# Kernel optimization log

Measured on AMD Instinct MI355X. Metric: run time of the kernel, lower is better.

Reference implementation:

```python
import jax, jax.numpy as jnp
import numpy as np

SEQ_LEN = 4096
D_IN = 2048
D_OUT = 2048
DROPOUT_P = 0.5


def setup_inputs() -> dict:
    key = jax.random.key(0)
    kx, kq, kk, kv = jax.random.split(key, 4)
    return {
        "x": jax.random.normal(kx, (SEQ_LEN, D_IN), dtype=jnp.float32),
        "W_query": jax.random.uniform(kq, (D_IN, D_OUT), dtype=jnp.float32),
        "W_key": jax.random.uniform(kk, (D_IN, D_OUT), dtype=jnp.float32),
        "W_value": jax.random.uniform(kv, (D_IN, D_OUT), dtype=jnp.float32),
    }


def reference(x, W_query, W_key, W_value):
    # projections: [S, d_in] @ [d_in, d_out] -> [S, d_out]
    queries = x @ W_query
    keys = x @ W_key
    values = x @ W_value
    # full score matrix [S, S]
    attn_scores = queries @ keys.T
    S = attn_scores.shape[0]
    causal_mask = jnp.triu(jnp.ones((S, S), dtype=bool), k=1)
    masked = jnp.where(causal_mask, -jnp.inf, attn_scores)
    scale = jnp.sqrt(jnp.asarray(keys.shape[-1], dtype=masked.dtype))
    attn_weights = jax.nn.softmax(masked / scale, axis=1)
    # dropout p=0.5 (train mode), inverted scaling, deterministic key
    keep = jax.random.bernoulli(jax.random.key(42), 1.0 - DROPOUT_P, attn_weights.shape)
    attn_weights = jnp.where(keep, attn_weights / (1.0 - DROPOUT_P), 0.0)
    context_vec = attn_weights @ values  # [S, d_out]
    return context_vec
```

## Files before the change

### kernel.cpp

```cpp
#include <hip/hip_runtime.h>
#include <cstdint>
#include <cstddef>
#include <cmath>

#define SEQ 4096
#define DM  2048

typedef unsigned int u32;
typedef unsigned short u16;
typedef __attribute__((ext_vector_type(8))) short bf16x8;
typedef __attribute__((ext_vector_type(4))) float f32x4;
typedef __attribute__((ext_vector_type(16))) float f32x16;

__device__ __forceinline__ u16 f2bf(float f) {
  u32 u = __float_as_uint(f);
  return (u16)((u + 0x7FFFu + ((u >> 16) & 1u)) >> 16);
}
__device__ __forceinline__ float bf2f(u16 h) { return __uint_as_float(((u32)h) << 16); }

__device__ __forceinline__ u32 rotl32(u32 x, int r) { return (x << r) | (x >> (32 - r)); }

__device__ __forceinline__ void tf2x32(u32 c0, u32 c1, u32& o0, u32& o1) {
  const u32 k0 = 0u, k1 = 42u, k2 = 0x1BD11BDAu ^ 0u ^ 42u;
  u32 x0 = c0 + k0;
  u32 x1 = c1 + k1;
#define TFR(r) { x0 += x1; x1 = rotl32(x1, (r)); x1 ^= x0; }
  TFR(13) TFR(15) TFR(26) TFR(6)   x0 += k1; x1 += k2 + 1u;
  TFR(17) TFR(29) TFR(16) TFR(24)  x0 += k2; x1 += k0 + 2u;
  TFR(13) TFR(15) TFR(26) TFR(6)   x0 += k0; x1 += k1 + 3u;
  TFR(17) TFR(29) TFR(16) TFR(24)  x0 += k1; x1 += k2 + 4u;
  TFR(13) TFR(15) TFR(26) TFR(6)   x0 += k2; x1 += k0 + 5u;
#undef TFR
  o0 = x0; o1 = x1;
}

__device__ __forceinline__ bool dropout_keep(u32 idx) {
  u32 a, b; tf2x32(0u, idx, a, b);
  return (((a ^ b) & 0x80000000u) == 0u);
}

__device__ __forceinline__ void g2l16(const void* g, void* l) {
  __builtin_amdgcn_global_load_lds((const __attribute__((address_space(1))) u32*)g,
                                   (__attribute__((address_space(3))) u32*)l, 16, 0, 0);
}

#define MFMA16(a, b, c) __builtin_amdgcn_mfma_f32_16x16x32_bf16(a, b, c, 0, 0, 0)
#define MFMA32(a, b, c) __builtin_amdgcn_mfma_f32_32x32x16_bf16(a, b, c, 0, 0, 0)


__device__ __forceinline__ void gemm_core(
    const u16* __restrict__ Ah, const u16* __restrict__ Bh,
    int lda, int ldb, int rowBlock, int colBlock, int kmax,
    f32x4 (&acc)[4][4], u16* smem)
{
  u16* Als = smem;
  u16* Bls = smem + 8192;
  const int tid  = threadIdx.x;
  const int wid  = tid >> 6;
  const int lane = tid & 63;
  const int wr   = (wid & 1) << 6;
  const int wc   = (wid >> 1) << 6;
  const int lrow = lane & 15;
  const int lk   = (((lane >> 4) ^ ((lrow >> 1) & 3)) << 3);
  const int srow = wid * 32 + (lane >> 2);
  const int skol = (((lane & 3) ^ ((lane >> 3) & 3)) << 3);

  const f32x4 zero = {0.f, 0.f, 0.f, 0.f};
#pragma unroll
  for (int i = 0; i < 4; ++i)
#pragma unroll
    for (int j = 0; j < 4; ++j) acc[i][j] = zero;

  for (int kb = 0; kb < kmax; kb += 64) {
#pragma unroll
    for (int h = 0; h < 2; ++h)
#pragma unroll
      for (int t = 0; t < 2; ++t) {
        const size_t ga = (size_t)(rowBlock + srow + t * 16) * lda + kb + h * 32 + skol;
        const size_t gb = (size_t)(colBlock + srow + t * 16) * ldb + kb + h * 32 + skol;
        const int lo = h * 4096 + (wid * 32 + t * 16) * 32;
        g2l16(Ah + ga, &Als[lo]);
        g2l16(Bh + gb, &Bls[lo]);
      }
    __syncthreads();

#pragma unroll
    for (int h = 0; h < 2; ++h) {
      bf16x8 ah[4], bh[4];
#pragma unroll
      for (int r = 0; r < 4; ++r) {
        ah[r] = *(const bf16x8*)&Als[h * 4096 + (wr + r * 16 + lrow) * 32 + lk];
        bh[r] = *(const bf16x8*)&Bls[h * 4096 + (wc + r * 16 + lrow) * 32 + lk];
      }
#pragma unroll
      for (int r = 0; r < 4; ++r)
#pragma unroll
        for (int c = 0; c < 4; ++c)
          acc[r][c] = MFMA16(ah[r], bh[c], acc[r][c]);
    }
    __syncthreads();
  }
}

__global__ __launch_bounds__(256) void k_split_all(
    const float* __restrict__ X, u16* __restrict__ Xh, u16* __restrict__ Xl,
    const float* __restrict__ Wq, const float* __restrict__ Wk, const float* __restrict__ Wv,
    u16* __restrict__ Wqh, u16* __restrict__ Wql,
    u16* __restrict__ Wkh, u16* __restrict__ Wkl, u16* __restrict__ Wvh) {
  __shared__ float t[64][65];
  const int bid = blockIdx.x;
  const int tid = threadIdx.x;
  const int wid = tid >> 6, lane = tid & 63;

  if (bid < 4096) {
    const int kt16 = bid & 127;
    const int rt32 = (bid >> 7) * 4 + wid;
    const int row = rt32 * 32 + (lane & 31);
    const int col = kt16 * 16 + ((lane >> 5) << 3);
    const float* src = X + (size_t)row * DM + col;
    const float4 v0 = *(const float4*)src;
    const float4 v1 = *(const float4*)(src + 4);
    float v[8] = {v0.x, v0.y, v0.z, v0.w, v1.x, v1.y, v1.z, v1.w};
    u16 h[8], l[8];
#pragma unroll
    for (int j = 0; j < 8; ++j) {
      h[j] = f2bf(v[j]);
      l[j] = f2bf(v[j] - bf2f(h[j]));
    }
    u16* hp = Xh + (size_t)row * DM + col;
    *(ushort4*)hp = *(ushort4*)&h[0];
    *(ushort4*)(hp + 4) = *(ushort4*)&h[4];
    u16* lp = Xl + (((size_t)rt32 * 128 + kt16) * 64 + lane) * 8;
    *(ushort4*)lp = *(ushort4*)&l[0];
    *(ushort4*)(lp + 4) = *(ushort4*)&l[4];
    return;
  }

  const int r = bid - 4096;
  const int z = r >> 10;
  const int rem = r & 1023;
  const int n0 = (rem & 31) * 64, k0 = (rem >> 5) * 64;
  const float* W = (z == 0) ? Wq : (z == 1) ? Wk : Wv;
  u16* Oh = (z == 0) ? Wqh : (z == 1) ? Wkh : Wvh;
  u16* Ol = (z == 0) ? Wql : Wkl;
  const int tx = tid & 63, ty = tid >> 6;
#pragma unroll
  for (int i = 0; i < 16; ++i)
    t[ty * 16 + i][tx] = W[(size_t)(k0 + ty * 16 + i) * DM + n0 + tx];
  __syncthreads();
  {
    const int nl = tid >> 2, kc = (tid & 3) * 16;
    u16 h[16];
#pragma unroll
    for (int i = 0; i < 16; ++i) h[i] = f2bf(t[kc + i][nl]);
    u16* hp = Oh + (size_t)(n0 + nl) * DM + k0 + kc;
#pragma unroll
    for (int i = 0; i < 4; ++i) *(ushort4*)(hp + i * 4) = *(ushort4*)&h[i * 4];
  }
  if (z < 2) {
#pragma unroll
    for (int tt = 0; tt < 2; ++tt) {
      const int idx = wid * 2 + tt;
      const int rt = idx >> 2, kt = idx & 3;
      const int nl = rt * 32 + (lane & 31);
      const int kc = kt * 16 + ((lane >> 5) << 3);
      u16 l[8];
#pragma unroll
      for (int j = 0; j < 8; ++j) {
        const float v = t[kc + j][nl];
        l[j] = f2bf(v - bf2f(f2bf(v)));
      }
      const int rtg = (n0 >> 5) + rt, ktg = (k0 >> 4) + kt;
      u16* lp = Ol + (((size_t)rtg * (DM / 16) + ktg) * 64 + lane) * 8;
      *(ushort4*)lp = *(ushort4*)&l[0];
      *(ushort4*)(lp + 4) = *(ushort4*)&l[4];
    }
  }
}

__global__ __launch_bounds__(512, 2) void k_proj_qk(
    const u16* __restrict__ Xh, const u16* __restrict__ Xl,
    const u16* __restrict__ Wqh, const u16* __restrict__ Wql,
    const u16* __restrict__ Wkh, const u16* __restrict__ Wkl,
    u16* __restrict__ Qh, u16* __restrict__ Ql,
    u16* __restrict__ Kh, u16* __restrict__ Kl, float rscaleQ)
{
  __shared__ __align__(16) u16 smem[65536];
  const int z = blockIdx.z;
  const u16* __restrict__ Bw = z ? Wkh : Wqh;
  const u16* __restrict__ Bl = z ? Wkl : Wql;
  u16* __restrict__ Oh = z ? Kh : Qh;
  u16* __restrict__ Ol = z ? Kl : Ql;
  const float rs = z ? 1.0f : rscaleQ;

  const int rowBlock = blockIdx.y * 256;
  const int colBlock = blockIdx.x * 256;
  const int tid  = threadIdx.x;
  const int wid  = tid >> 6, lane = tid & 63;
  const int wm   = wid >> 2, wn = wid & 3;
  const int l31  = lane & 31, lh = lane >> 5;
  const int srow = tid >> 2, schunk = tid & 3;
  const int sko  = ((schunk ^ ((srow >> 1) & 3)) << 3);
  const int rkey = (l31 >> 1) & 3;

  f32x16 acc[4][2];
  {
    const f32x16 z16 = {0.f,0.f,0.f,0.f,0.f,0.f,0.f,0.f,0.f,0.f,0.f,0.f,0.f,0.f,0.f,0.f};
#pragma unroll
    for (int r = 0; r < 4; ++r)
#pragma unroll
      for (int c = 0; c < 2; ++c) acc[r][c] = z16;
  }

#define P_STG_AHI(pp) g2l16(Xh + (size_t)(rowBlock + (pp)*128 + srow) * DM + kbn + sko, \
                            &smem[bufN + (pp)*4096 + tid*8]);
#define P_STG_BHI(pp) g2l16(Bw + (size_t)(colBlock + (pp)*128 + srow) * DM + kbn + sko, \
                            &smem[bufN + 8192 + (pp)*4096 + tid*8]);
#define P_STG_ALO(ss) { const int idx_ = (ss)*8 + wid; \
    g2l16(Xl + ((size_t)((rowBlock >> 5) + (idx_ >> 1)) * 128 + (kbn >> 4) + (idx_ & 1)) * 512 + lane*8, \
          &smem[bufN + 16384 + idx_*512 + lane*8]); }
#define P_STG_BLO(ss) { const int idx_ = (ss)*8 + wid; \
    g2l16(Bl + ((size_t)((colBlock >> 5) + (idx_ >> 1)) * 128 + (kbn >> 4) + (idx_ & 1)) * 512 + lane*8, \
          &smem[bufN + 24576 + idx_*512 + lane*8]); }

#define P_PHASE(qq) { \
    bf16x8 ah[4], bh[2], al[4], bl[2]; \
    const int cl_ = (qq)*2 + lh; \
    _Pragma("unroll") for (int r_ = 0; r_ < 4; ++r_) \
      ah[r_] = *(const bf16x8*)&smem[bufC + ((wm*128 + r_*32 + l31) << 5) + ((cl_ ^ rkey) << 3)]; \
    _Pragma("unroll") for (int c_ = 0; c_ < 2; ++c_) \
      bh[c_] = *(const bf16x8*)&smem[bufC + 8192 + ((wn*64 + c_*32 + l31) << 5) + ((cl_ ^ rkey) << 3)]; \
    _Pragma("unroll") for (int r_ = 0; r_ < 4; ++r_) \
      al[r_] = *(const bf16x8*)&smem[bufC + 16384 + ((wm*4 + r_)*2 + (qq))*512 + lane*8]; \
    _Pragma("unroll") for (int c_ = 0; c_ < 2; ++c_) \
      bl[c_] = *(const bf16x8*)&smem[bufC + 24576 + ((wn*2 + c_)*2 + (qq))*512 + lane*8]; \
    __builtin_amdgcn_s_setprio(1); \
    _Pragma("unroll") for (int r_ = 0; r_ < 4; ++r_) \
      _Pragma("unroll") for (int c_ = 0; c_ < 2; ++c_) { \
        acc[r_][c_] = MFMA32(ah[r_], bh[c_], acc[r_][c_]); \
        acc[r_][c_] = MFMA32(ah[r_], bl[c_], acc[r_][c_]); \
        acc[r_][c_] = MFMA32(al[r_], bh[c_], acc[r_][c_]); } \
    __builtin_amdgcn_s_setprio(0); }

  {
    const size_t kbn = 0; const int bufN = 0;
    P_STG_AHI(0) P_STG_AHI(1) P_STG_BHI(0) P_STG_BHI(1)
    P_STG_ALO(0) P_STG_ALO(1) P_STG_BLO(0) P_STG_BLO(1)
  }
  asm volatile("s_waitcnt vmcnt(0)" ::: "memory");
  __builtin_amdgcn_s_barrier();

  for (int t = 0; t < 64; ++t) {
    const int bufC = (t & 1) << 15;
    const int bufN = bufC ^ 32768;
    const size_t kbn = (size_t)(t + 1) * 32;
    if (t < 63) { P_STG_AHI(0) P_STG_AHI(1) P_STG_BHI(0) P_STG_BHI(1) }
    __builtin_amdgcn_sched_barrier(0);
    P_PHASE(0)
    if (t < 63) { P_STG_ALO(0) P_STG_ALO(1) P_STG_BLO(0) P_STG_BLO(1) }
    __builtin_amdgcn_sched_barrier(0);
    P_PHASE(1)
    asm volatile("s_waitcnt vmcnt(0)" ::: "memory");
    __builtin_amdgcn_s_barrier();
  }
#undef P_PHASE
#undef P_STG_BLO
#undef P_STG_ALO
#undef P_STG_BHI
#undef P_STG_AHI

  __syncthreads();
  u16* scr = smem + wid * 8192;
  const int r0g = rowBlock + wm * 128;
  const int c0g = colBlock + wn * 64;
#pragma unroll
  for (int r = 0; r < 4; ++r)
#pragma unroll
    for (int c = 0; c < 2; ++c) {
      const int colL = c * 32 + l31;
#pragma unroll
      for (int g = 0; g < 4; ++g)
#pragma unroll
        for (int e = 0; e < 4; ++e) {
          const int rowL = r * 32 + 8 * g + 4 * lh + e;
          const float v = acc[r][c][g * 4 + e] * rs;
          const u16 h = f2bf(v);
          Oh[(size_t)(r0g + rowL) * DM + c0g + colL] = h;
          scr[rowL * 64 + (((colL >> 3) ^ (rowL & 7)) << 3) + (colL & 7)] =
              f2bf(v - bf2f(h));
        }
    }
  asm volatile("s_waitcnt lgkmcnt(0)" ::: "memory");
  __builtin_amdgcn_sched_barrier(0);
#pragma unroll
  for (int rt = 0; rt < 4; ++rt)
#pragma unroll
    for (int kt = 0; kt < 4; ++kt) {
      const int rowL = rt * 32 + l31;
      const int cl2 = kt * 2 + lh;
      const bf16x8 v = *(const bf16x8*)&scr[rowL * 64 + ((cl2 ^ (rowL & 7)) << 3)];
      const int rtg = (rowBlock >> 5) + wm * 4 + rt;
      const int ktg = (colBlock >> 4) + wn * 4 + kt;
      *(bf16x8*)(Ol + (((size_t)rtg * 128 + ktg) * 64 + lane) * 8) = v;
    }
}

__global__ __launch_bounds__(512, 2) void k_proj_v(
    const u16* __restrict__ Xh, const u16* __restrict__ Wvh, u16* __restrict__ Vt)
{
  __shared__ __align__(16) u16 smem[49152];
  const int rowBlock = blockIdx.y * 256;
  const int colBlock = blockIdx.x * 128;
  const int tid  = threadIdx.x;
  const int wid  = tid >> 6, lane = tid & 63;
  const int wm   = wid >> 1, wn = wid & 1;
  const int l31  = lane & 31, lh = lane >> 5;
  const int srow = tid >> 2, schunk = tid & 3;
  const int sko  = ((schunk ^ ((srow >> 1) & 3)) << 3);
  const int rkey = (l31 >> 1) & 3;

  f32x16 acc[2][2];
  {
    const f32x16 z16 = {0.f,0.f,0.f,0.f,0.f,0.f,0.f,0.f,0.f,0.f,0.f,0.f,0.f,0.f,0.f,0.f};
#pragma unroll
    for (int r = 0; r < 2; ++r)
#pragma unroll
      for (int c = 0; c < 2; ++c) acc[r][c] = z16;
  }

#define V_STGA(hh, pp) g2l16(Xh + (size_t)(rowBlock + (pp)*128 + srow) * DM + kbn + (hh)*32 + sko, \
                             &smem[bufN + (hh)*8192 + (pp)*4096 + tid*8]);
#define V_STGB(hh)     g2l16(Wvh + (size_t)(colBlock + srow) * DM + kbn + (hh)*32 + sko, \
                             &smem[bufN + 16384 + (hh)*4096 + tid*8]);

#define V_PH(qq, STMT) { \
    __builtin_amdgcn_sched_barrier(0); \
    STMT; \
    bf16x8 ah[2], bh[2]; \
    const int cl_ = ((qq) & 1) * 2 + lh; \
    const int hx_ = (qq) >> 1; \
    _Pragma("unroll") for (int r_ = 0; r_ < 2; ++r_) \
      ah[r_] = *(const bf16x8*)&smem[bufC + ((hx_*256 + wm*64 + r_*32 + l31) << 5) + ((cl_ ^ rkey) << 3)]; \
    _Pragma("unroll") for (int c_ = 0; c_ < 2; ++c_) \
      bh[c_] = *(const bf16x8*)&smem[bufC + 16384 + ((hx_*128 + wn*64 + c_*32 + l31) << 5) + ((cl_ ^ rkey) << 3)]; \
    __builtin_amdgcn_s_setprio(1); \
    _Pragma("unroll") for (int r_ = 0; r_ < 2; ++r_) \
      _Pragma("unroll") for (int c_ = 0; c_ < 2; ++c_) \
        acc[r_][c_] = MFMA32(ah[r_], bh[c_], acc[r_][c_]); \
    __builtin_amdgcn_s_setprio(0); }

  {
    const size_t kbn = 0; const int bufN = 0;
    V_STGA(0,0) V_STGA(0,1) V_STGA(1,0) V_STGA(1,1) V_STGB(0) V_STGB(1)
  }
  asm volatile("s_waitcnt vmcnt(0)" ::: "memory");
  __builtin_amdgcn_s_barrier();

  for (int t = 0; t < 32; ++t) {
    const int bufC = (t & 1) * 24576;
    const int bufN = bufC ^ 24576;
    const size_t kbn = (size_t)(t + 1) * 64;
    const bool more = (t < 31);
    V_PH(0, if (more) { V_STGA(0,0) V_STGA(0,1) V_STGB(0) })
    V_PH(1, if (more) { V_STGA(1,0) V_STGA(1,1) V_STGB(1) })
    V_PH(2, ;)
    V_PH(3, ;)
    asm volatile("s_waitcnt vmcnt(0)" ::: "memory");
    __builtin_amdgcn_s_barrier();
  }
#undef V_PH
#undef V_STGB
#undef V_STGA

  const int vr0 = rowBlock + wm * 64;
#pragma unroll
  for (int r = 0; r < 2; ++r)
#pragma unroll
    for (int c = 0; c < 2; ++c) {
      const int col = colBlock + wn * 64 + c * 32 + l31;
#pragma unroll
      for (int g = 0; g < 4; ++g) {
        ushort4 pk;
        pk.x = f2bf(acc[r][c][g * 4 + 0]);
        pk.y = f2bf(acc[r][c][g * 4 + 1]);
        pk.z = f2bf(acc[r][c][g * 4 + 2]);
        pk.w = f2bf(acc[r][c][g * 4 + 3]);
        *(ushort4*)(Vt + (size_t)col * SEQ + vr0 + r * 32 + 8 * g + 4 * lh) = pk;
      }
    }
}

__global__ __launch_bounds__(512, 2) void k_scores(
    const u16* __restrict__ Qh, const u16* __restrict__ Ql,
    const u16* __restrict__ Kh, const u16* __restrict__ Kl, float* __restrict__ S)
{
  __shared__ __align__(16) u16 smem[49152];
  const int bid = blockIdx.x;
  int by = (int)((sqrtf(4.0f * (float)bid + 1.0f) - 1.0f) * 0.5f);
  while ((by + 1) * (by + 2) <= bid) ++by;
  while (by * (by + 1) > bid) --by;
  const int bx = bid - by * (by + 1);
  const int rowBlock = by * 256, colBlock = bx * 128;

  const int tid  = threadIdx.x;
  const int wid  = tid >> 6, lane = tid & 63;
  const int wm   = wid >> 1, wn = wid & 1;
  const int l31  = lane & 31, lh = lane >> 5;
  const int srow = tid >> 2, schunk = tid & 3;
  const int sko  = ((schunk ^ ((srow >> 1) & 3)) << 3);
  const int rkey = (l31 >> 1) & 3;

  f32x16 acc[2][2];
  {
    const f32x16 z16 = {0.f,0.f,0.f,0.f,0.f,0.f,0.f,0.f,0.f,0.f,0.f,0.f,0.f,0.f,0.f,0.f};
#pragma unroll
    for (int r = 0; r < 2; ++r)
#pragma unroll
      for (int c = 0; c < 2; ++c) acc[r][c] = z16;
  }

#define S_STG_AHI(pp) g2l16(Qh + (size_t)(rowBlock + (pp)*128 + srow) * DM + kbn + sko, \
                            &smem[bufN + (pp)*4096 + tid*8]);
#define S_STG_BHI     g2l16(Kh + (size_t)(colBlock + srow) * DM + kbn + sko, \
                            &smem[bufN + 8192 + tid*8]);
#define S_STG_ALO(ss) { const int idx_ = (ss)*8 + wid; \
    g2l16(Ql + ((size_t)((rowBlock >> 5) + (idx_ >> 1)) * 128 + (kbn >> 4) + (idx_ & 1)) * 512 + lane*8, \
          &smem[bufN + 12288 + idx_*512 + lane*8]); }
#define S_STG_BLO     { const int idx_ = wid; \
    g2l16(Kl + ((size_t)((colBlock >> 5) + (idx_ >> 1)) * 128 + (kbn >> 4) + (idx_ & 1)) * 512 + lane*8, \
          &smem[bufN + 20480 + idx_*512 + lane*8]); }

#define S_PHASE(qq) { \
    bf16x8 ah[2], bh[2], al[2], bl[2]; \
    const int cl_ = (qq)*2 + lh; \
    _Pragma("unroll") for (int r_ = 0; r_ < 2; ++r_) \
      ah[r_] = *(const bf16x8*)&smem[bufC + ((wm*64 + r_*32 + l31) << 5) + ((cl_ ^ rkey) << 3)]; \
    _Pragma("unroll") for (int c_ = 0; c_ < 2; ++c_) \
      bh[c_] = *(const bf16x8*)&smem[bufC + 8192 + ((wn*64 + c_*32 + l31) << 5) + ((cl_ ^ rkey) << 3)]; \
    _Pragma("unroll") for (int r_ = 0; r_ < 2; ++r_) \
      al[r_] = *(const bf16x8*)&smem[bufC + 12288 + ((wm*2 + r_)*2 + (qq))*512 + lane*8]; \
    _Pragma("unroll") for (int c_ = 0; c_ < 2; ++c_) \
      bl[c_] = *(const bf16x8*)&smem[bufC + 20480 + ((wn*2 + c_)*2 + (qq))*512 + lane*8]; \
    __builtin_amdgcn_s_setprio(1); \
    _Pragma("unroll") for (int r_ = 0; r_ < 2; ++r_) \
      _Pragma("unroll") for (int c_ = 0; c_ < 2; ++c_) { \
        acc[r_][c_] = MFMA32(ah[r_], bh[c_], acc[r_][c_]); \
        acc[r_][c_] = MFMA32(ah[r_], bl[c_], acc[r_][c_]); \
        acc[r_][c_] = MFMA32(al[r_], bh[c_], acc[r_][c_]); } \
    __builtin_amdgcn_s_setprio(0); }

  {
    const size_t kbn = 0; const int bufN = 0;
    S_STG_AHI(0) S_STG_AHI(1) S_STG_BHI
    S_STG_ALO(0) S_STG_ALO(1) S_STG_BLO
  }
  asm volatile("s_waitcnt vmcnt(0)" ::: "memory");
  __builtin_amdgcn_s_barrier();

  for (int t = 0; t < 64; ++t) {
    const int bufC = (t & 1) * 24576;
    const int bufN = bufC ^ 24576;
    const size_t kbn = (size_t)(t + 1) * 32;
    if (t < 63) { S_STG_AHI(0) S_STG_AHI(1) S_STG_BHI }
    __builtin_amdgcn_sched_barrier(0);
    S_PHASE(0)
    if (t < 63) { S_STG_ALO(0) S_STG_ALO(1) S_STG_BLO }
    __builtin_amdgcn_sched_barrier(0);
    S_PHASE(1)
    asm volatile("s_waitcnt vmcnt(0)" ::: "memory");
    __builtin_amdgcn_s_barrier();
  }
#undef S_PHASE
#undef S_STG_BLO
#undef S_STG_ALO
#undef S_STG_BHI
#undef S_STG_AHI

  const int r0 = rowBlock + wm * 64, c0 = colBlock + wn * 64;
#pragma unroll
  for (int r = 0; r < 2; ++r)
#pragma unroll
    for (int c = 0; c < 2; ++c) {
      const int col = c0 + c * 32 + l31;
#pragma unroll
      for (int g = 0; g < 4; ++g)
#pragma unroll
        for (int e = 0; e < 4; ++e) {
          const int row = r0 + r * 32 + 8 * g + 4 * lh + e;
          S[(size_t)row * SEQ + col] = acc[r][c][g * 4 + e];
        }
    }
}

__global__ __launch_bounds__(256) void k_softmax_dropout(const float* __restrict__ S,
                                                         u16* __restrict__ P) {
  const int row = blockIdx.x;
  const int n = row + 1;
  const int nt = (n + 1023) >> 10;
  const int tid = threadIdx.x;
  __shared__ float buf[SEQ];
  __shared__ float red[4];
  __shared__ float bcast;
  const float* srow = S + (size_t)row * SEQ;

  float lmax = -INFINITY;
  for (int t = 0; t < nt; ++t) {
    int j4 = tid + t * 256;
    float4 v = *(const float4*)(srow + (size_t)j4 * 4);
    int b = j4 * 4;
    float x0 = (b + 0 < n) ? v.x : -INFINITY;
    float x1 = (b + 1 < n) ? v.y : -INFINITY;
    float x2 = (b + 2 < n) ? v.z : -INFINITY;
    float x3 = (b + 3 < n) ? v.w : -INFINITY;
    buf[b + 0] = x0; buf[b + 1] = x1; buf[b + 2] = x2; buf[b + 3] = x3;
    lmax = fmaxf(lmax, fmaxf(fmaxf(x0, x1), fmaxf(x2, x3)));
  }
  for (int off = 32; off > 0; off >>= 1) lmax = fmaxf(lmax, __shfl_down(lmax, off, 64));
  if ((tid & 63) == 0) red[tid >> 6] = lmax;
  __syncthreads();
  if (tid == 0) bcast = fmaxf(fmaxf(red[0], red[1]), fmaxf(red[2], red[3]));
  __syncthreads();
  const float m = bcast;

  float lsum = 0.f;
  for (int t = 0; t < nt; ++t) {
    int b = (tid + t * 256) * 4;
    float e0 = expf(buf[b + 0] - m);
    float e1 = expf(buf[b + 1] - m);
    float e2 = expf(buf[b + 2] - m);
    float e3 = expf(buf[b + 3] - m);
    buf[b + 0] = e0; buf[b + 1] = e1; buf[b + 2] = e2; buf[b + 3] = e3;
    lsum += (e0 + e1) + (e2 + e3);
  }
  for (int off = 32; off > 0; off >>= 1) lsum += __shfl_down(lsum, off, 64);
  if ((tid & 63) == 0) red[tid >> 6] = lsum;
  __syncthreads();
  if (tid == 0) bcast = (red[0] + red[1]) + (red[2] + red[3]);
  __syncthreads();
  const float total = bcast;

  u16* prow = P + (size_t)row * SEQ;
  const int zeroEnd = ((row >> 7) + 1) << 7;
  for (int j = tid; j < zeroEnd; j += 256) {
    float out = 0.f;
    if (j < n) {
      const float w = buf[j] / total;
      out = dropout_keep((u32)(row * SEQ + j)) ? w * 2.0f : 0.f;
    }
    prow[j] = f2bf(out);
  }
}

__global__ __launch_bounds__(256) void k_pv(const u16* __restrict__ P,
                                            const u16* __restrict__ Vt,
                                            float* __restrict__ O) {
  __shared__ __align__(16) u16 smem[16384];
  const int by = (SEQ / 128 - 1) - blockIdx.y;
  f32x4 acc[4][4];
  gemm_core(P, Vt, SEQ, SEQ, by * 128, blockIdx.x * 128, (by + 1) * 128, acc, smem);

  const int lane = threadIdx.x & 63, wid = threadIdx.x >> 6;
  const int r0 = by * 128 + ((wid & 1) << 6) + ((lane >> 4) << 2);
  const int c0 = blockIdx.x * 128 + ((wid >> 1) << 6) + (lane & 15);
#pragma unroll
  for (int r = 0; r < 4; ++r)
#pragma unroll
    for (int c = 0; c < 4; ++c)
#pragma unroll
      for (int e = 0; e < 4; ++e)
        O[(size_t)(r0 + r * 16 + e) * DM + (c0 + c * 16)] = acc[r][c][e];
}

extern "C" void kernel_launch(void* const* d_in, const int* in_sizes, int n_in,
                              void* d_out, int out_size, void* d_ws, size_t ws_size,
                              hipStream_t stream) {
  const float* x  = (const float*)d_in[0];
  const float* Wq = (const float*)d_in[1];
  const float* Wk = (const float*)d_in[2];
  const float* Wv = (const float*)d_in[3];

  const size_t PL = (size_t)SEQ * DM;
  const size_t WL = (size_t)DM * DM;
  u16* base = (u16*)d_ws;
  u16* Qh = base;
  u16* Ql = Qh + PL;
  u16* Kh = Ql + PL;
  u16* Kl = Kh + PL;
  u16* Vt = Kl + PL;
  u16* P  = base;
  u16* regA = Vt + PL;
  u16* Xh  = regA;
  u16* Xl  = Xh + PL;
  u16* Wqh = Xl + PL;
  u16* Wql = Wqh + WL;
  u16* Wkh = Wql + WL;
  u16* Wkl = Wkh + WL;
  u16* Wvh = Wkl + WL;
  float* S = (float*)regA;

  const float rscale = 1.0f / sqrtf(2048.0f);
  k_split_all<<<dim3(4096 + 3 * 1024), dim3(256), 0, stream>>>(
      x, Xh, Xl, Wq, Wk, Wv, Wqh, Wql, Wkh, Wkl, Wvh);
  k_proj_qk<<<dim3(DM / 256, SEQ / 256, 2), dim3(512), 0, stream>>>(
      Xh, Xl, Wqh, Wql, Wkh, Wkl, Qh, Ql, Kh, Kl, rscale);
  k_proj_v<<<dim3(DM / 128, SEQ / 256), dim3(512), 0, stream>>>(Xh, Wvh, Vt);
  k_scores<<<dim3(272), dim3(512), 0, stream>>>(Qh, Ql, Kh, Kl, S);
  k_softmax_dropout<<<dim3(SEQ), dim3(256), 0, stream>>>(S, P);
  k_pv<<<dim3(DM / 128, SEQ / 128), dim3(256), 0, stream>>>(P, Vt, (float*)d_out);
}
```

Baseline: 610.4 us.

## Fuse V projection into scores launch, compact causal S, stream lo-parts from global

The V projection and the causal score GEMM now share one launch, with blocks beyond the score range computing V, so the two independent workloads can overlap and fill the GPU. The score matrix is stored in a packed lower-triangular layout indexed by 128-row bands, which shrinks the fp32 scratch footprint and lets it live in the Xl region. The QK projection is also restructured to stage only the high bf16 halves in shared memory with a deeper k-step, while the low halves are loaded straight from global memory into registers with double buffering. This cuts LDS traffic but adds direct global loads inside the MFMA loop.

```diff
diff --git a/kernel.cpp b/kernel.cpp
--- a/kernel.cpp
+++ b/kernel.cpp
@@ -17,6 +17,11 @@
   return (u16)((u + 0x7FFFu + ((u >> 16) & 1u)) >> 16);
 }
 __device__ __forceinline__ float bf2f(u16 h) { return __uint_as_float(((u32)h) << 16); }
+
+__device__ __forceinline__ size_t s_base(int row) {
+  const int b = row >> 7;
+  return (size_t)8192 * b * (b + 1) + (size_t)128 * (row & 127) * (b + 1);
+}
 
 __device__ __forceinline__ u32 rotl32(u32 x, int r) { return (x << r) | (x >> (32 - r)); }
 
@@ -202,6 +207,8 @@
   const int srow = tid >> 2, schunk = tid & 3;
   const int sko  = ((schunk ^ ((srow >> 1) & 3)) << 3);
   const int rkey = (l31 >> 1) & 3;
+  const int rtA0 = (rowBlock >> 5) + wm * 4;
+  const int rtB0 = (colBlock >> 5) + wn * 2;
 
   f32x16 acc[4][2];
   {
@@ -211,63 +218,65 @@
 #pragma unroll
       for (int c = 0; c < 2; ++c) acc[r][c] = z16;
   }
-
-#define P_STG_AHI(pp) g2l16(Xh + (size_t)(rowBlock + (pp)*128 + srow) * DM + kbn + sko, \
-                            &smem[bufN + (pp)*4096 + tid*8]);
-#define P_STG_BHI(pp) g2l16(Bw + (size_t)(colBlock + (pp)*128 + srow) * DM + kbn + sko, \
-                            &smem[bufN + 8192 + (pp)*4096 + tid*8]);
-#define P_STG_ALO(ss) { const int idx_ = (ss)*8 + wid; \
-    g2l16(Xl + ((size_t)((rowBlock >> 5) + (idx_ >> 1)) * 128 + (kbn >> 4) + (idx_ & 1)) * 512 + lane*8, \
-          &smem[bufN + 16384 + idx_*512 + lane*8]); }
-#define P_STG_BLO(ss) { const int idx_ = (ss)*8 + wid; \
-    g2l16(Bl + ((size_t)((colBlock >> 5) + (idx_ >> 1)) * 128 + (kbn >> 4) + (idx_ & 1)) * 512 + lane*8, \
-          &smem[bufN + 24576 + idx_*512 + lane*8]); }
-
-#define P_PHASE(qq) { \
-    bf16x8 ah[4], bh[2], al[4], bl[2]; \
-    const int cl_ = (qq)*2 + lh; \
+  bf16x8 alo0[4], blo0[2], alo1[4], blo1[2];
+
+#define QK_STG(hh, pp) { \
+    g2l16(Xh + (size_t)(rowBlock + (pp)*128 + srow) * DM + kbn + (hh)*32 + sko, \
+          &smem[bufN + (hh)*8192 + (pp)*4096 + tid*8]); \
+    g2l16(Bw + (size_t)(colBlock + (pp)*128 + srow) * DM + kbn + (hh)*32 + sko, \
+          &smem[bufN + 16384 + (hh)*8192 + (pp)*4096 + tid*8]); }
+
+#define QK_LO(AV, BV, kt) { \
+    const int kk_ = (kt); \
     _Pragma("unroll") for (int r_ = 0; r_ < 4; ++r_) \
-      ah[r_] = *(const bf16x8*)&smem[bufC + ((wm*128 + r_*32 + l31) << 5) + ((cl_ ^ rkey) << 3)]; \
+      AV[r_] = *(const bf16x8*)(Xl + (((size_t)(rtA0 + r_) * 128 + kk_) * 64 + lane) * 8); \
     _Pragma("unroll") for (int c_ = 0; c_ < 2; ++c_) \
-      bh[c_] = *(const bf16x8*)&smem[bufC + 8192 + ((wn*64 + c_*32 + l31) << 5) + ((cl_ ^ rkey) << 3)]; \
+      BV[c_] = *(const bf16x8*)(Bl + (((size_t)(rtB0 + c_) * 128 + kk_) * 64 + lane) * 8); }
+
+#define QK_PH(qq, ALC, BLC, ALN, BLN, STMT, ktn) { \
+    __builtin_amdgcn_sched_barrier(0); \
+    QK_LO(ALN, BLN, ktn); \
+    __builtin_amdgcn_sched_barrier(0); \
+    STMT; \
+    bf16x8 ah[4], bh[2]; \
+    const int cl_ = ((qq) & 1) * 2 + lh; \
+    const int hx_ = (qq) >> 1; \
     _Pragma("unroll") for (int r_ = 0; r_ < 4; ++r_) \
-      al[r_] = *(const bf16x8*)&smem[bufC + 16384 + ((wm*4 + r_)*2 + (qq))*512 + lane*8]; \
+      ah[r_] = *(const bf16x8*)&smem[bufC + ((hx_*256 + wm*128 + r_*32 + l31) << 5) + ((cl_ ^ rkey) << 3)]; \
     _Pragma("unroll") for (int c_ = 0; c_ < 2; ++c_) \
-      bl[c_] = *(const bf16x8*)&smem[bufC + 24576 + ((wn*2 + c_)*2 + (qq))*512 + lane*8]; \
+      bh[c_] = *(const bf16x8*)&smem[bufC + 16384 + ((hx_*256 + wn*64 + c_*32 + l31) << 5) + ((cl_ ^ rkey) << 3)]; \
     __builtin_amdgcn_s_setprio(1); \
     _Pragma("unroll") for (int r_ = 0; r_ < 4; ++r_) \
       _Pragma("unroll") for (int c_ = 0; c_ < 2; ++c_) { \
         acc[r_][c_] = MFMA32(ah[r_], bh[c_], acc[r_][c_]); \
-        acc[r_][c_] = MFMA32(ah[r_], bl[c_], acc[r_][c_]); \
-        acc[r_][c_] = MFMA32(al[r_], bh[c_], acc[r_][c_]); } \
+        acc[r_][c_] = MFMA32(ah[r_], BLC[c_], acc[r_][c_]); \
+        acc[r_][c_] = MFMA32(ALC[r_], bh[c_], acc[r_][c_]); } \
     __builtin_amdgcn_s_setprio(0); }
 
   {
     const size_t kbn = 0; const int bufN = 0;
-    P_STG_AHI(0) P_STG_AHI(1) P_STG_BHI(0) P_STG_BHI(1)
-    P_STG_ALO(0) P_STG_ALO(1) P_STG_BLO(0) P_STG_BLO(1)
-  }
+    QK_STG(0,0) QK_STG(0,1) QK_STG(1,0) QK_STG(1,1)
+  }
+  QK_LO(alo0, blo0, 0);
   asm volatile("s_waitcnt vmcnt(0)" ::: "memory");
   __builtin_amdgcn_s_barrier();
 
-  for (int t = 0; t < 64; ++t) {
+  for (int t = 0; t < 32; ++t) {
     const int bufC = (t & 1) << 15;
     const int bufN = bufC ^ 32768;
-    const size_t kbn = (size_t)(t + 1) * 32;
-    if (t < 63) { P_STG_AHI(0) P_STG_AHI(1) P_STG_BHI(0) P_STG_BHI(1) }
-    __builtin_amdgcn_sched_barrier(0);
-    P_PHASE(0)
-    if (t < 63) { P_STG_ALO(0) P_STG_ALO(1) P_STG_BLO(0) P_STG_BLO(1) }
-    __builtin_amdgcn_sched_barrier(0);
-    P_PHASE(1)
+    const size_t kbn = (size_t)(t + 1) * 64;
+    const bool more = (t < 31);
+    const int g4 = t * 4;
+    QK_PH(0, alo0, blo0, alo1, blo1, if (more) { QK_STG(0,0) QK_STG(0,1) }, g4 + 1)
+    QK_PH(1, alo1, blo1, alo0, blo0, if (more) { QK_STG(1,0) QK_STG(1,1) }, g4 + 2)
+    QK_PH(2, alo0, blo0, alo1, blo1, ;, g4 + 3)
+    QK_PH(3, alo1, blo1, alo0, blo0, ;, (g4 + 4 < 128 ? g4 + 4 : 127))
     asm volatile("s_waitcnt vmcnt(0)" ::: "memory");
     __builtin_amdgcn_s_barrier();
   }
-#undef P_PHASE
-#undef P_STG_BLO
-#undef P_STG_ALO
-#undef P_STG_BHI
-#undef P_STG_AHI
+#undef QK_PH
+#undef QK_LO
+#undef QK_STG
 
   __syncthreads();
   u16* scr = smem + wid * 8192;
@@ -305,96 +314,11 @@
     }
 }
 
-__global__ __launch_bounds__(512, 2) void k_proj_v(
-    const u16* __restrict__ Xh, const u16* __restrict__ Wvh, u16* __restrict__ Vt)
+__device__ __forceinline__ void scores_body(
+    const u16* __restrict__ Qh, const u16* __restrict__ Ql,
+    const u16* __restrict__ Kh, const u16* __restrict__ Kl,
+    float* __restrict__ S, u16* smem)
 {
-  __shared__ __align__(16) u16 smem[49152];
-  const int rowBlock = blockIdx.y * 256;
-  const int colBlock = blockIdx.x * 128;
-  const int tid  = threadIdx.x;
-  const int wid  = tid >> 6, lane = tid & 63;
-  const int wm   = wid >> 1, wn = wid & 1;
-  const int l31  = lane & 31, lh = lane >> 5;
-  const int srow = tid >> 2, schunk = tid & 3;
-  const int sko  = ((schunk ^ ((srow >> 1) & 3)) << 3);
-  const int rkey = (l31 >> 1) & 3;
-
-  f32x16 acc[2][2];
-  {
-    const f32x16 z16 = {0.f,0.f,0.f,0.f,0.f,0.f,0.f,0.f,0.f,0.f,0.f,0.f,0.f,0.f,0.f,0.f};
-#pragma unroll
-    for (int r = 0; r < 2; ++r)
-#pragma unroll
-      for (int c = 0; c < 2; ++c) acc[r][c] = z16;
-  }
-
-#define V_STGA(hh, pp) g2l16(Xh + (size_t)(rowBlock + (pp)*128 + srow) * DM + kbn + (hh)*32 + sko, \
-                             &smem[bufN + (hh)*8192 + (pp)*4096 + tid*8]);
-#define V_STGB(hh)     g2l16(Wvh + (size_t)(colBlock + srow) * DM + kbn + (hh)*32 + sko, \
-                             &smem[bufN + 16384 + (hh)*4096 + tid*8]);
-
-#define V_PH(qq, STMT) { \
-    __builtin_amdgcn_sched_barrier(0); \
-    STMT; \
-    bf16x8 ah[2], bh[2]; \
-    const int cl_ = ((qq) & 1) * 2 + lh; \
-    const int hx_ = (qq) >> 1; \
-    _Pragma("unroll") for (int r_ = 0; r_ < 2; ++r_) \
-      ah[r_] = *(const bf16x8*)&smem[bufC + ((hx_*256 + wm*64 + r_*32 + l31) << 5) + ((cl_ ^ rkey) << 3)]; \
-    _Pragma("unroll") for (int c_ = 0; c_ < 2; ++c_) \
-      bh[c_] = *(const bf16x8*)&smem[bufC + 16384 + ((hx_*128 + wn*64 + c_*32 + l31) << 5) + ((cl_ ^ rkey) << 3)]; \
-    __builtin_amdgcn_s_setprio(1); \
-    _Pragma("unroll") for (int r_ = 0; r_ < 2; ++r_) \
-      _Pragma("unroll") for (int c_ = 0; c_ < 2; ++c_) \
-        acc[r_][c_] = MFMA32(ah[r_], bh[c_], acc[r_][c_]); \
-    __builtin_amdgcn_s_setprio(0); }
-
-  {
-    const size_t kbn = 0; const int bufN = 0;
-    V_STGA(0,0) V_STGA(0,1) V_STGA(1,0) V_STGA(1,1) V_STGB(0) V_STGB(1)
-  }
-  asm volatile("s_waitcnt vmcnt(0)" ::: "memory");
-  __builtin_amdgcn_s_barrier();
-
-  for (int t = 0; t < 32; ++t) {
-    const int bufC = (t & 1) * 24576;
-    const int bufN = bufC ^ 24576;
-    const size_t kbn = (size_t)(t + 1) * 64;
-    const bool more = (t < 31);
-    V_PH(0, if (more) { V_STGA(0,0) V_STGA(0,1) V_STGB(0) })
-    V_PH(1, if (more) { V_STGA(1,0) V_STGA(1,1) V_STGB(1) })
-    V_PH(2, ;)
-    V_PH(3, ;)
-    asm volatile("s_waitcnt vmcnt(0)" ::: "memory");
-    __builtin_amdgcn_s_barrier();
-  }
-#undef V_PH
-#undef V_STGB
-#undef V_STGA
-
-  const int vr0 = rowBlock + wm * 64;
-#pragma unroll
-  for (int r = 0; r < 2; ++r)
-#pragma unroll
-    for (int c = 0; c < 2; ++c) {
-      const int col = colBlock + wn * 64 + c * 32 + l31;
-#pragma unroll
-      for (int g = 0; g < 4; ++g) {
-        ushort4 pk;
-        pk.x = f2bf(acc[r][c][g * 4 + 0]);
-        pk.y = f2bf(acc[r][c][g * 4 + 1]);
-        pk.z = f2bf(acc[r][c][g * 4 + 2]);
-        pk.w = f2bf(acc[r][c][g * 4 + 3]);
-        *(ushort4*)(Vt + (size_t)col * SEQ + vr0 + r * 32 + 8 * g + 4 * lh) = pk;
-      }
-    }
-}
-
-__global__ __launch_bounds__(512, 2) void k_scores(
-    const u16* __restrict__ Qh, const u16* __restrict__ Ql,
-    const u16* __restrict__ Kh, const u16* __restrict__ Kl, float* __restrict__ S)
-{
-  __shared__ __align__(16) u16 smem[49152];
   const int bid = blockIdx.x;
   int by = (int)((sqrtf(4.0f * (float)bid + 1.0f) - 1.0f) * 0.5f);
   while ((by + 1) * (by + 2) <= bid) ++by;
@@ -487,9 +411,110 @@
 #pragma unroll
         for (int e = 0; e < 4; ++e) {
           const int row = r0 + r * 32 + 8 * g + 4 * lh + e;
-          S[(size_t)row * SEQ + col] = acc[r][c][g * 4 + e];
+          if ((col >> 7) <= (row >> 7))
+            S[s_base(row) + col] = acc[r][c][g * 4 + e];
         }
     }
+}
+
+__device__ __forceinline__ void projv_body(
+    const u16* __restrict__ Xh, const u16* __restrict__ Wvh,
+    u16* __restrict__ Vt, int vbid, u16* smem)
+{
+  const int rowBlock = (vbid >> 4) * 256;
+  const int colBlock = (vbid & 15) * 128;
+  const int tid  = threadIdx.x;
+  const int wid  = tid >> 6, lane = tid & 63;
+  const int wm   = wid >> 1, wn = wid & 1;
+  const int l31  = lane & 31, lh = lane >> 5;
+  const int srow = tid >> 2, schunk = tid & 3;
+  const int sko  = ((schunk ^ ((srow >> 1) & 3)) << 3);
+  const int rkey = (l31 >> 1) & 3;
+
+  f32x16 acc[2][2];
+  {
+    const f32x16 z16 = {0.f,0.f,0.f,0.f,0.f,0.f,0.f,0.f,0.f,0.f,0.f,0.f,0.f,0.f,0.f,0.f};
+#pragma unroll
+    for (int r = 0; r < 2; ++r)
+#pragma unroll
+      for (int c = 0; c < 2; ++c) acc[r][c] = z16;
+  }
+
+#define V_STGA(hh, pp) g2l16(Xh + (size_t)(rowBlock + (pp)*128 + srow) * DM + kbn + (hh)*32 + sko, \
+                             &smem[bufN + (hh)*8192 + (pp)*4096 + tid*8]);
+#define V_STGB(hh)     g2l16(Wvh + (size_t)(colBlock + srow) * DM + kbn + (hh)*32 + sko, \
+                             &smem[bufN + 16384 + (hh)*4096 + tid*8]);
+
+#define V_PH(qq, STMT) { \
+    __builtin_amdgcn_sched_barrier(0); \
+    STMT; \
+    bf16x8 ah[2], bh[2]; \
+    const int cl_ = ((qq) & 1) * 2 + lh; \
+    const int hx_ = (qq) >> 1; \
+    _Pragma("unroll") for (int r_ = 0; r_ < 2; ++r_) \
+      ah[r_] = *(const bf16x8*)&smem[bufC + ((hx_*256 + wm*64 + r_*32 + l31) << 5) + ((cl_ ^ rkey) << 3)]; \
+    _Pragma("unroll") for (int c_ = 0; c_ < 2; ++c_) \
+      bh[c_] = *(const bf16x8*)&smem[bufC + 16384 + ((hx_*128 + wn*64 + c_*32 + l31) << 5) + ((cl_ ^ rkey) << 3)]; \
+    __builtin_amdgcn_s_setprio(1); \
+    _Pragma("unroll") for (int r_ = 0; r_ < 2; ++r_) \
+      _Pragma("unroll") for (int c_ = 0; c_ < 2; ++c_) \
+        acc[r_][c_] = MFMA32(ah[r_], bh[c_], acc[r_][c_]); \
+    __builtin_amdgcn_s_setprio(0); }
+
+  {
+    const size_t kbn = 0; const int bufN = 0;
+    V_STGA(0,0) V_STGA(0,1) V_STGA(1,0) V_STGA(1,1) V_STGB(0) V_STGB(1)
+  }
+  asm volatile("s_waitcnt vmcnt(0)" ::: "memory");
+  __builtin_amdgcn_s_barrier();
+
+  for (int t = 0; t < 32; ++t) {
+    const int bufC = (t & 1) * 24576;
+    const int bufN = bufC ^ 24576;
+    const size_t kbn = (size_t)(t + 1) * 64;
+    const bool more = (t < 31);
+    V_PH(0, if (more) { V_STGA(0,0) V_STGA(0,1) V_STGB(0) })
+    V_PH(1, if (more) { V_STGA(1,0) V_STGA(1,1) V_STGB(1) })
+    V_PH(2, ;)
+    V_PH(3, ;)
+    asm volatile("s_waitcnt vmcnt(0)" ::: "memory");
+    __builtin_amdgcn_s_barrier();
+  }
+#undef V_PH
+#undef V_STGB
+#undef V_STGA
+
+  const int vr0 = rowBlock + wm * 64;
+#pragma unroll
+  for (int r = 0; r < 2; ++r)
+#pragma unroll
+    for (int c = 0; c < 2; ++c) {
+      const int col = colBlock + wn * 64 + c * 32 + l31;
+#pragma unroll
+      for (int g = 0; g < 4; ++g) {
+        ushort4 pk;
+        pk.x = f2bf(acc[r][c][g * 4 + 0]);
+        pk.y = f2bf(acc[r][c][g * 4 + 1]);
+        pk.z = f2bf(acc[r][c][g * 4 + 2]);
+        pk.w = f2bf(acc[r][c][g * 4 + 3]);
+        *(ushort4*)(Vt + (size_t)col * SEQ + vr0 + r * 32 + 8 * g + 4 * lh) = pk;
+      }
+    }
+}
+
+__global__ __launch_bounds__(512, 2) void k_scores_v(
+    const u16* __restrict__ Qh, const u16* __restrict__ Ql,
+    const u16* __restrict__ Kh, const u16* __restrict__ Kl,
+    float* __restrict__ S,
+    const u16* __restrict__ Xh, const u16* __restrict__ Wvh,
+    u16* __restrict__ Vt)
+{
+  __shared__ __align__(16) u16 smem[49152];
+  if (blockIdx.x < 272) {
+    scores_body(Qh, Ql, Kh, Kl, S, smem);
+  } else {
+    projv_body(Xh, Wvh, Vt, blockIdx.x - 272, smem);
+  }
 }
 
 __global__ __launch_bounds__(256) void k_softmax_dropout(const float* __restrict__ S,
@@ -501,7 +526,7 @@
   __shared__ float buf[SEQ];
   __shared__ float red[4];
   __shared__ float bcast;
-  const float* srow = S + (size_t)row * SEQ;
+  const float* srow = S + s_base(row);
 
   float lmax = -INFINITY;
   for (int t = 0; t < nt; ++t) {
@@ -596,15 +621,15 @@
   u16* Wkh = Wql + WL;
   u16* Wkl = Wkh + WL;
   u16* Wvh = Wkl + WL;
-  float* S = (float*)regA;
+  float* S = (float*)Xl;
 
   const float rscale = 1.0f / sqrtf(2048.0f);
   k_split_all<<<dim3(4096 + 3 * 1024), dim3(256), 0, stream>>>(
       x, Xh, Xl, Wq, Wk, Wv, Wqh, Wql, Wkh, Wkl, Wvh);
   k_proj_qk<<<dim3(DM / 256, SEQ / 256, 2), dim3(512), 0, stream>>>(
       Xh, Xl, Wqh, Wql, Wkh, Wkl, Qh, Ql, Kh, Kl, rscale);
-  k_proj_v<<<dim3(DM / 128, SEQ / 256), dim3(512), 0, stream>>>(Xh, Wvh, Vt);
-  k_scores<<<dim3(272), dim3(512), 0, stream>>>(Qh, Ql, Kh, Kl, S);
+  k_scores_v<<<dim3(272 + 256), dim3(512), 0, stream>>>(
+      Qh, Ql, Kh, Kl, S, Xh, Wvh, Vt);
   k_softmax_dropout<<<dim3(SEQ), dim3(256), 0, stream>>>(S, P);
   k_pv<<<dim3(DM / 128, SEQ / 128), dim3(256), 0, stream>>>(P, Vt, (float*)d_out);
 }
```

Measured after the change: 583.5 us, median of 2. 1.05x faster.
